# Kernel tuning notes

Hardware: AMD Instinct MI355X
Metric: run time of the kernel (lower is better)

## Reference

```python
import jax, jax.numpy as jnp
import numpy as np

N, E, R, F_IN, F_OUT = 50000, 800000, 6, 128, 128


def setup_inputs() -> dict:
    key = jax.random.key(0)
    ks = jax.random.split(key, 9)
    return {
        "node_h": jax.random.normal(ks[0], (N, F_IN), jnp.float32),
        "weight": jax.random.normal(ks[1], (R, F_IN, F_OUT), jnp.float32) * 0.05,
        "att1": jax.random.normal(ks[2], (F_OUT, 1), jnp.float32),
        "att2": jax.random.normal(ks[3], (F_OUT, 1), jnp.float32),
        "Wc": jax.random.normal(ks[4], (F_OUT, 2 * F_OUT), jnp.float32) * 0.05,
        "bc": jnp.zeros((F_OUT,), jnp.float32),
        "edge_src": jax.random.randint(ks[5], (E,), 0, N, dtype=jnp.int64) if jax.config.jax_enable_x64 else jax.random.randint(ks[5], (E,), 0, N),
        "edge_dst": jax.random.randint(ks[6], (E,), 0, N),
        "edge_rel": jax.random.randint(ks[7], (E,), 0, R),
    }


def reference(node_h, weight, att1, att2, Wc, bc, edge_src, edge_dst, edge_rel):
    n = node_h.shape[0]
    # combined (relation, dst) segment id -> replaces dense per-relation adjacency
    seg = edge_rel * n + edge_dst
    # per-relation incoming degree of each dst node: [R, N]
    deg = jax.ops.segment_sum(
        jnp.ones(edge_src.shape, jnp.float32), seg, num_segments=R * n
    ).reshape(R, n)
    # per-relation transformed features hrd[r] = h @ W[r]: [R, N, O]
    hrd = jnp.einsum('nf,rfo->rno', node_h, weight)
    # per-edge message = hrd[rel_e, src_e]: [E, O]
    msg = hrd[edge_rel, edge_src]
    # scatter-sum into (rel, dst) then normalize by 1/(1 + deg_r(dst))
    agg = jax.ops.segment_sum(msg, seg, num_segments=R * n).reshape(R, n, F_OUT)
    hrs = agg / (1.0 + deg)[:, :, None]
    op = jnp.transpose(hrs, (1, 0, 2))  # [N, R, O]
    # two attention heads: softmax over the relation axis
    s1 = jax.nn.softmax(op @ att1, axis=1)  # [N, R, 1]
    s2 = jax.nn.softmax(op @ att2, axis=1)
    h_comb = jnp.concatenate([op * s1, op * s2], axis=-1)  # [N, R, 2O]
    h5 = h_comb @ Wc.T + bc  # attention_concat linear: [N, R, O]
    h = jnp.sum(h5, axis=1)  # sum over relations: [N, O]
    return (h, weight)
```

## Files before the change

kernel.cpp:

```cpp
#include <hip/hip_runtime.h>

#define NN 50000
#define NE 800000
#define NR 6
#define FD 128
#define NS (NN * NR)
#define MB ((NS + 1023) / 1024)

typedef __attribute__((ext_vector_type(8))) short bf16x8;
typedef __attribute__((ext_vector_type(4))) float f32x4;

__device__ __forceinline__ unsigned short f2bf(float x) {
    unsigned u = __float_as_uint(x);
    u += 0x7FFFu + ((u >> 16) & 1u);
    return (unsigned short)(u >> 16);
}
__device__ __forceinline__ unsigned pack2bf(float lo, float hi) {
    return (unsigned)f2bf(lo) | ((unsigned)f2bf(hi) << 16);
}
__device__ __forceinline__ float bf_lo(unsigned u) { return __uint_as_float(u << 16); }
__device__ __forceinline__ float bf_hi(unsigned u) { return __uint_as_float(u & 0xFFFF0000u); }

__global__ __launch_bounds__(256) void k_cast(
    const float* __restrict__ node_h, unsigned* __restrict__ nh2)
{
    int i = (blockIdx.x * 256 + threadIdx.x) * 8;
    float4 a = *(const float4*)(node_h + i);
    float4 b = *(const float4*)(node_h + i + 4);
    uint4 o;
    o.x = pack2bf(a.x, a.y); o.y = pack2bf(a.z, a.w);
    o.z = pack2bf(b.x, b.y); o.w = pack2bf(b.z, b.w);
    *(uint4*)(nh2 + i / 2) = o;
}

__global__ __launch_bounds__(256) void k_hist(
    const int* __restrict__ edst, const int* __restrict__ erel,
    int* __restrict__ cnt)
{
    int e = blockIdx.x * 256 + threadIdx.x;
    if (e < NE) atomicAdd(cnt + edst[e] * NR + erel[e], 1);
}

__global__ __launch_bounds__(256) void k_bsum(
    const int* __restrict__ cnt, int* __restrict__ bsum)
{
    __shared__ int red[256];
    const int b = blockIdx.x, t = threadIdx.x;
    int idx0 = b * 1024 + t * 4;
    int4 c = *(const int4*)(cnt + idx0);
    int s = 0;
    if (idx0 + 0 < NS) s += c.x;
    if (idx0 + 1 < NS) s += c.y;
    if (idx0 + 2 < NS) s += c.z;
    if (idx0 + 3 < NS) s += c.w;
    red[t] = s;
    __syncthreads();
    for (int off = 128; off > 0; off >>= 1) {
        if (t < off) red[t] += red[t + off];
        __syncthreads();
    }
    if (t == 0) bsum[b] = red[0];
}

__global__ __launch_bounds__(512) void k_scanb(
    const int* __restrict__ bsum, int* __restrict__ bpre)
{
    __shared__ int s[512];
    const int t = threadIdx.x;
    int v = (t < MB) ? bsum[t] : 0;
    s[t] = v;
    __syncthreads();
    for (int off = 1; off < 512; off <<= 1) {
        int x = (t >= off) ? s[t - off] : 0;
        __syncthreads();
        if (t >= off) s[t] += x;
        __syncthreads();
    }
    bpre[t] = s[t] - v;
}

__global__ __launch_bounds__(256) void k_scan3(
    const int* __restrict__ cnt, const int* __restrict__ bpre,
    int* __restrict__ offs, int* __restrict__ cursor)
{
    __shared__ int partial[256];
    const int b = blockIdx.x, t = threadIdx.x;
    int idx0 = b * 1024 + t * 4;
    int4 c = *(const int4*)(cnt + idx0);
    if (idx0 + 0 >= NS) c.x = 0;
    if (idx0 + 1 >= NS) c.y = 0;
    if (idx0 + 2 >= NS) c.z = 0;
    if (idx0 + 3 >= NS) c.w = 0;
    int tsum = c.x + c.y + c.z + c.w;
    partial[t] = tsum;
    __syncthreads();
    for (int off = 1; off < 256; off <<= 1) {
        int x = (t >= off) ? partial[t - off] : 0;
        __syncthreads();
        if (t >= off) partial[t] += x;
        __syncthreads();
    }
    int base = bpre[b] + partial[t] - tsum;
    int4 o;
    o.x = base;
    o.y = base + c.x;
    o.z = base + c.x + c.y;
    o.w = base + c.x + c.y + c.z;
    if (idx0 + 3 < NS) {
        *(int4*)(offs + idx0) = o;
        *(int4*)(cursor + idx0) = o;
    } else {
        int v[4] = {o.x, o.y, o.z, o.w};
        for (int k = 0; k < 4; ++k)
            if (idx0 + k < NS) { offs[idx0 + k] = v[k]; cursor[idx0 + k] = v[k]; }
    }
    if (b == 0 && t == 0) offs[NS] = NE;
}

__global__ __launch_bounds__(256) void k_place(
    const int* __restrict__ esrc, const int* __restrict__ edst,
    const int* __restrict__ erel, int* __restrict__ cursor,
    int* __restrict__ eidx)
{
    int e = blockIdx.x * 256 + threadIdx.x;
    if (e >= NE) return;
    int seg = edst[e] * NR + erel[e];
    int pos = atomicAdd(cursor + seg, 1);
    eidx[pos] = esrc[e];
}

__global__ __launch_bounds__(256) void k_prep_w(
    const float* __restrict__ weight,
    const float* __restrict__ att1, const float* __restrict__ att2,
    float* __restrict__ w1, float* __restrict__ w2)
{
    __shared__ float a1s[FD], a2s[FD];
    const int r = blockIdx.x;
    const int t = threadIdx.x;
    if (t < FD) { a1s[t] = att1[t]; a2s[t] = att2[t]; }
    __syncthreads();
    int f = t & 127;
    const float* av = (t < FD) ? a1s : a2s;
    float* wo = (t < FD) ? w1 : w2;
    const float* Wrow = weight + ((size_t)r * FD + f) * FD;
    float acc = 0.f;
#pragma unroll 8
    for (int o = 0; o < FD; ++o) acc += Wrow[o] * av[o];
    wo[r * FD + f] = acc;
}

__global__ __launch_bounds__(256) void k_prep_U(
    const float* __restrict__ weight, const float* __restrict__ Wc,
    short* __restrict__ Upk)
{
    __shared__ float As[64 * 65];
    __shared__ float Bs[64 * 132];
    const int h  = blockIdx.y / NR;
    const int r  = blockIdx.y % NR;
    const int f0 = blockIdx.x * 64;
    const int t  = threadIdx.x;
    const int tm = t & 15, tn = t >> 4;

    float acc[4][8];
#pragma unroll
    for (int i = 0; i < 4; ++i)
#pragma unroll
        for (int j = 0; j < 8; ++j) acc[i][j] = 0.f;

    for (int kt = 0; kt < 2; ++kt) {
#pragma unroll
        for (int i = 0; i < 4; ++i) {
            int flat = i * 1024 + t * 4;
            int row = flat >> 6, k = flat & 63;
            float4 v = *(const float4*)(weight + ((size_t)r * FD + f0 + row) * FD + kt * 64 + k);
            float* p = As + row * 65 + k;
            p[0] = v.x; p[1] = v.y; p[2] = v.z; p[3] = v.w;
        }
#pragma unroll
        for (int i = 0; i < 8; ++i) {
            int flat4 = i * 256 + t;
            int o = flat4 >> 4, j4 = flat4 & 15;
            float4 v = *(const float4*)(Wc + (size_t)o * 256 + h * FD + kt * 64 + j4 * 4);
            float* p = Bs + (j4 * 4) * 132 + o;
            p[0] = v.x; p[132] = v.y; p[264] = v.z; p[396] = v.w;
        }
        __syncthreads();
#pragma unroll 4
        for (int k = 0; k < 64; ++k) {
            float aa[4];
#pragma unroll
            for (int i = 0; i < 4; ++i) aa[i] = As[(4 * tm + i) * 65 + k];
            float4 blo = *(const float4*)(Bs + k * 132 + 8 * tn);
            float4 bhi = *(const float4*)(Bs + k * 132 + 8 * tn + 4);
            float bb[8] = {blo.x, blo.y, blo.z, blo.w, bhi.x, bhi.y, bhi.z, bhi.w};
#pragma unroll
            for (int i = 0; i < 4; ++i)
#pragma unroll
                for (int j = 0; j < 8; ++j) acc[i][j] += aa[i] * bb[j];
        }
        __syncthreads();
    }

#pragma unroll
    for (int i = 0; i < 4; ++i)
#pragma unroll
        for (int j = 0; j < 8; ++j) {
            int f = f0 + 4 * tm + i, o = 8 * tn + j;
            int kstep = f >> 5, g = (f >> 3) & 3, jj = f & 7;
            int nt = o >> 4, ln = g * 16 + (o & 15);
            size_t sidx = ((((size_t)(h * NR + r) * 4 + kstep) * 8 + nt) * 64 + ln) * 8 + jj;
            Upk[sidx] = (short)f2bf(acc[i][j]);
        }
}

__global__ __launch_bounds__(256) void k_agg(
    const unsigned* __restrict__ nh2,
    const int* __restrict__ offs,
    const int* __restrict__ eidx,
    const float* __restrict__ w1v, const float* __restrict__ w2v,
    unsigned* __restrict__ aggp,
    float* __restrict__ s1o, float* __restrict__ s2o)
{
    const int t = threadIdx.x;
    const int lane = t & 63;
    const int d = blockIdx.x * 4 + (t >> 6);
    if (d >= NN) return;

    float w1l[NR], w1h[NR], w2l[NR], w2h[NR];
#pragma unroll
    for (int r = 0; r < NR; ++r) {
        float2 a = *(const float2*)(w1v + r * FD + 2 * lane);
        float2 b = *(const float2*)(w2v + r * FD + 2 * lane);
        w1l[r] = a.x; w1h[r] = a.y; w2l[r] = b.x; w2h[r] = b.y;
    }

    int bnd[NR + 1];
#pragma unroll
    for (int i = 0; i <= NR; ++i) bnd[i] = offs[d * NR + i];

    float p1[NR], p2[NR];
#pragma unroll
    for (int r = 0; r < NR; ++r) {
        const int beg = bnd[r], end = bnd[r + 1];
        float ax = 0.f, ay = 0.f;
        unsigned vcur = 0;
        if (beg < end) vcur = nh2[(size_t)eidx[beg] * 64 + lane];
        for (int j = beg; j < end; ++j) {
            unsigned v = vcur;
            if (j + 1 < end) vcur = nh2[(size_t)eidx[j + 1] * 64 + lane];
            ax += bf_lo(v); ay += bf_hi(v);
        }
        float sc = 1.0f / (1.0f + (float)(end - beg));
        ax *= sc; ay *= sc;
        aggp[((size_t)r * NN + d) * 64 + lane] = pack2bf(ax, ay);
        p1[r] = ax * w1l[r] + ay * w1h[r];
        p2[r] = ax * w2l[r] + ay * w2h[r];
    }

#pragma unroll
    for (int off = 32; off > 0; off >>= 1)
#pragma unroll
        for (int r = 0; r < NR; ++r) {
            p1[r] += __shfl_xor(p1[r], off, 64);
            p2[r] += __shfl_xor(p2[r], off, 64);
        }

    float m1 = p1[0], m2 = p2[0];
#pragma unroll
    for (int r = 1; r < NR; ++r) { m1 = fmaxf(m1, p1[r]); m2 = fmaxf(m2, p2[r]); }
    float e1[NR], e2[NR], d1 = 0.f, d2 = 0.f;
#pragma unroll
    for (int r = 0; r < NR; ++r) {
        e1[r] = __expf(p1[r] - m1); d1 += e1[r];
        e2[r] = __expf(p2[r] - m2); d2 += e2[r];
    }
    d1 = 1.0f / d1; d2 = 1.0f / d2;
    if (lane == 0) {
#pragma unroll
        for (int r = 0; r < NR; ++r) {
            s1o[d * NR + r] = e1[r] * d1;
            s2o[d * NR + r] = e2[r] * d2;
        }
    }
}

__global__ __launch_bounds__(256, 4) void k_fused(
    const unsigned* __restrict__ aggp,
    const float* __restrict__ s1, const float* __restrict__ s2,
    const short* __restrict__ Upk,
    const float* __restrict__ bc,
    float* __restrict__ out)
{
    __shared__ short Al[64 * 128];
    __shared__ float sl[2 * 64 * NR];
    const int n0 = blockIdx.x * 64;
    const int t = threadIdx.x;
    const int lane = t & 63;
    const int w = t >> 6;

    for (int i = t; i < 2 * 64 * NR; i += 256) {
        int h = i / (64 * NR);
        int rr = i % (64 * NR);
        int row = rr / NR, r = rr % NR;
        int n = n0 + row;
        float v = 0.f;
        if (n < NN) v = (h ? s2 : s1)[(size_t)n * NR + r];
        sl[i] = v;
    }

    f32x4 acc[8];
#pragma unroll
    for (int nt = 0; nt < 8; ++nt) acc[nt] = (f32x4){0.f, 0.f, 0.f, 0.f};

    const int m = w * 16 + (lane & 15);
    const int g = lane >> 4;

    for (int r = 0; r < NR; ++r) {
        __syncthreads();
        {
            int row = t >> 2, kq = t & 3;
            int n = n0 + row;
            const unsigned* src = aggp + ((size_t)r * NN + n) * 64 + kq * 16;
#pragma unroll
            for (int c = 0; c < 4; ++c) {
                uint4 v = make_uint4(0, 0, 0, 0);
                if (n < NN) v = *(const uint4*)(src + c * 4);
                int ks = kq * 32 + c * 8;
                int addr = row * 128 + (ks ^ ((row & 7) << 3));
                *(uint4*)&Al[addr] = v;
            }
        }
        __syncthreads();

#pragma unroll
        for (int h = 0; h < 2; ++h) {
            f32x4 ar[8];
#pragma unroll
            for (int nt = 0; nt < 8; ++nt) ar[nt] = (f32x4){0.f, 0.f, 0.f, 0.f};
#pragma unroll
            for (int kstep = 0; kstep < 4; ++kstep) {
                bf16x8 af = *(const bf16x8*)&Al[m * 128 + ((kstep * 32 + g * 8) ^ ((m & 7) << 3))];
                const short* Ub = Upk + (((size_t)(h * NR + r) * 4 + kstep) * 8) * 64 * 8 + lane * 8;
#pragma unroll
                for (int nt = 0; nt < 8; ++nt) {
                    bf16x8 bfr = *(const bf16x8*)(Ub + nt * 64 * 8);
                    ar[nt] = __builtin_amdgcn_mfma_f32_16x16x32_bf16(af, bfr, ar[nt], 0, 0, 0);
                }
            }
            float sv[4];
#pragma unroll
            for (int reg = 0; reg < 4; ++reg)
                sv[reg] = sl[h * 64 * NR + (w * 16 + (lane >> 4) * 4 + reg) * NR + r];
#pragma unroll
            for (int nt = 0; nt < 8; ++nt)
#pragma unroll
                for (int reg = 0; reg < 4; ++reg)
                    acc[nt][reg] += sv[reg] * ar[nt][reg];
        }
    }

    const int rowbase = n0 + w * 16 + (lane >> 4) * 4;
    const int col0 = lane & 15;
#pragma unroll
    for (int nt = 0; nt < 8; ++nt) {
        int col = nt * 16 + col0;
        float b6 = 6.0f * bc[col];
#pragma unroll
        for (int reg = 0; reg < 4; ++reg) {
            int n = rowbase + reg;
            if (n < NN) out[(size_t)n * FD + col] = acc[nt][reg] + b6;
        }
    }
}

extern "C" void kernel_launch(void* const* d_in, const int* in_sizes, int n_in,
                              void* d_out, int out_size, void* d_ws, size_t ws_size,
                              hipStream_t stream)
{
    const float* node_h = (const float*)d_in[0];
    const float* weight = (const float*)d_in[1];
    const float* att1   = (const float*)d_in[2];
    const float* att2   = (const float*)d_in[3];
    const float* Wc     = (const float*)d_in[4];
    const float* bc     = (const float*)d_in[5];
    const int* esrc = (const int*)d_in[6];
    const int* edst = (const int*)d_in[7];
    const int* erel = (const int*)d_in[8];
    float* out = (float*)d_out;

    char* wsp = (char*)d_ws;
    auto alloc = [&](size_t bytes) {
        char* p = wsp;
        wsp += (bytes + 255) & ~(size_t)255;
        return p;
    };
    unsigned* aggp = (unsigned*)alloc((size_t)NR * NN * 64 * 4);
    unsigned* nh2  = (unsigned*)alloc((size_t)NN * 64 * 4);
    short* Upk     = (short*)alloc((size_t)2 * NR * FD * FD * 2);
    float* w1      = (float*)alloc(NR * FD * 4);
    float* w2      = (float*)alloc(NR * FD * 4);
    float* s1      = (float*)alloc((size_t)NN * NR * 4);
    float* s2      = (float*)alloc((size_t)NN * NR * 4);
    int* offs      = (int*)alloc((size_t)(NS + 1 + 64) * 4);
    int* cursor    = (int*)alloc((size_t)(NS + 2048) * 4);
    int* bsum      = (int*)alloc(512 * 4);
    int* bpre      = (int*)alloc(512 * 4);
    int* eidx      = (int*)d_out;

    hipMemsetAsync(cursor, 0, (size_t)NS * sizeof(int), stream);

    k_hist<<<(NE + 255) / 256, 256, 0, stream>>>(edst, erel, cursor);
    k_bsum<<<MB, 256, 0, stream>>>(cursor, bsum);
    k_scanb<<<1, 512, 0, stream>>>(bsum, bpre);
    k_scan3<<<MB, 256, 0, stream>>>(cursor, bpre, offs, cursor);
    k_place<<<(NE + 255) / 256, 256, 0, stream>>>(esrc, edst, erel, cursor, eidx);

    k_cast<<<(NN * FD / 8 + 255) / 256, 256, 0, stream>>>(node_h, nh2);
    k_prep_w<<<NR, 256, 0, stream>>>(weight, att1, att2, w1, w2);
    k_prep_U<<<dim3(2, 2 * NR), 256, 0, stream>>>(weight, Wc, Upk);

    k_agg<<<(NN + 3) / 4, 256, 0, stream>>>(nh2, offs, eidx, w1, w2, aggp, s1, s2);

    k_fused<<<(NN + 63) / 64, 256, 0, stream>>>(aggp, s1, s2, Upk, bc, out);

    hipMemcpyAsync(out + (size_t)NN * FD, weight,
                   (size_t)NR * FD * FD * sizeof(float),
                   hipMemcpyDeviceToDevice, stream);
}
```

Measured before the change: 390.2 us.

## Split aggregation wavefront into 16-lane groups, one relation each, with 16-byte gathers

The aggregation kernel now splits each 64-lane wavefront into four 16-lane groups. Each group handles one relation, and six relations take two passes. Each lane gathers 16 bytes (8 bf16 features) per edge instead of 4 bytes, so relation segments are processed in parallel and memory requests are wider. The attention dot-product reduction shrinks to a 16-lane butterfly followed by broadcasts. In exchange, the second pass leaves half the lanes idle, each lane holds more registers, and the prefetch of the next source row is dropped.

```diff
diff --git a/kernel.cpp b/kernel.cpp
--- a/kernel.cpp
+++ b/kernel.cpp
@@ -223,47 +223,62 @@
 {
     const int t = threadIdx.x;
     const int lane = t & 63;
+    const int grp = lane >> 4;
+    const int fl  = lane & 15;
     const int d = blockIdx.x * 4 + (t >> 6);
     if (d >= NN) return;
 
-    float w1l[NR], w1h[NR], w2l[NR], w2h[NR];
-#pragma unroll
-    for (int r = 0; r < NR; ++r) {
-        float2 a = *(const float2*)(w1v + r * FD + 2 * lane);
-        float2 b = *(const float2*)(w2v + r * FD + 2 * lane);
-        w1l[r] = a.x; w1h[r] = a.y; w2l[r] = b.x; w2h[r] = b.y;
-    }
-
-    int bnd[NR + 1];
-#pragma unroll
-    for (int i = 0; i <= NR; ++i) bnd[i] = offs[d * NR + i];
+    float p1v[2], p2v[2];
+
+#pragma unroll
+    for (int pass = 0; pass < 2; ++pass) {
+        const int r = pass * 4 + grp;
+        float q1 = 0.f, q2 = 0.f;
+        if (r < NR) {
+            const int sbeg = offs[d * NR + r];
+            const int send = offs[d * NR + r + 1];
+            float a0 = 0.f, a1 = 0.f, a2 = 0.f, a3 = 0.f;
+            float a4 = 0.f, a5 = 0.f, a6 = 0.f, a7 = 0.f;
+            for (int j = sbeg; j < send; ++j) {
+                int s = eidx[j];
+                uint4 v = *(const uint4*)(nh2 + (size_t)s * 64 + fl * 4);
+                a0 += bf_lo(v.x); a1 += bf_hi(v.x);
+                a2 += bf_lo(v.y); a3 += bf_hi(v.y);
+                a4 += bf_lo(v.z); a5 += bf_hi(v.z);
+                a6 += bf_lo(v.w); a7 += bf_hi(v.w);
+            }
+            float sc = 1.0f / (1.0f + (float)(send - sbeg));
+            a0 *= sc; a1 *= sc; a2 *= sc; a3 *= sc;
+            a4 *= sc; a5 *= sc; a6 *= sc; a7 *= sc;
+            uint4 o;
+            o.x = pack2bf(a0, a1); o.y = pack2bf(a2, a3);
+            o.z = pack2bf(a4, a5); o.w = pack2bf(a6, a7);
+            *(uint4*)(aggp + ((size_t)r * NN + d) * 64 + fl * 4) = o;
+            float4 wa = *(const float4*)(w1v + r * FD + fl * 8);
+            float4 wb = *(const float4*)(w1v + r * FD + fl * 8 + 4);
+            float4 wc = *(const float4*)(w2v + r * FD + fl * 8);
+            float4 wd = *(const float4*)(w2v + r * FD + fl * 8 + 4);
+            q1 = a0 * wa.x + a1 * wa.y + a2 * wa.z + a3 * wa.w
+               + a4 * wb.x + a5 * wb.y + a6 * wb.z + a7 * wb.w;
+            q2 = a0 * wc.x + a1 * wc.y + a2 * wc.z + a3 * wc.w
+               + a4 * wd.x + a5 * wd.y + a6 * wd.z + a7 * wd.w;
+        }
+#pragma unroll
+        for (int off = 1; off < 16; off <<= 1) {
+            q1 += __shfl_xor(q1, off, 64);
+            q2 += __shfl_xor(q2, off, 64);
+        }
+        p1v[pass] = q1; p2v[pass] = q2;
+    }
 
     float p1[NR], p2[NR];
 #pragma unroll
-    for (int r = 0; r < NR; ++r) {
-        const int beg = bnd[r], end = bnd[r + 1];
-        float ax = 0.f, ay = 0.f;
-        unsigned vcur = 0;
-        if (beg < end) vcur = nh2[(size_t)eidx[beg] * 64 + lane];
-        for (int j = beg; j < end; ++j) {
-            unsigned v = vcur;
-            if (j + 1 < end) vcur = nh2[(size_t)eidx[j + 1] * 64 + lane];
-            ax += bf_lo(v); ay += bf_hi(v);
-        }
-        float sc = 1.0f / (1.0f + (float)(end - beg));
-        ax *= sc; ay *= sc;
-        aggp[((size_t)r * NN + d) * 64 + lane] = pack2bf(ax, ay);
-        p1[r] = ax * w1l[r] + ay * w1h[r];
-        p2[r] = ax * w2l[r] + ay * w2h[r];
-    }
-
-#pragma unroll
-    for (int off = 32; off > 0; off >>= 1)
-#pragma unroll
-        for (int r = 0; r < NR; ++r) {
-            p1[r] += __shfl_xor(p1[r], off, 64);
-            p2[r] += __shfl_xor(p2[r], off, 64);
-        }
+    for (int r = 0; r < 4; ++r) {
+        p1[r] = __shfl(p1v[0], r * 16, 64);
+        p2[r] = __shfl(p2v[0], r * 16, 64);
+    }
+    p1[4] = __shfl(p1v[1], 0, 64);  p1[5] = __shfl(p1v[1], 16, 64);
+    p2[4] = __shfl(p2v[1], 0, 64);  p2[5] = __shfl(p2v[1], 16, 64);
 
     float m1 = p1[0], m2 = p2[0];
 #pragma unroll
```

After: 355.1 us. 9.0% less time.
